# Kernel tuning notes

Hardware: AMD Instinct MI355X
Metric: run time of the kernel (lower is better)

Reference implementation:

```python
import jax, jax.numpy as jnp
import numpy as np

C = 192

def _dw_conv(x, w, k):
    # x: [B, C, H, W]; w: [C, 1, k, k]; depthwise => feature_group_count=C
    pad = k // 2
    return jax.lax.conv_general_dilated(
        x, w,
        window_strides=(1, 1),
        padding=[(pad, pad), (pad, pad)],
        dimension_numbers=("NCHW", "OIHW", "NCHW"),
        feature_group_count=x.shape[1],
    )

def setup_inputs() -> dict:
    key = jax.random.key(0)
    k1, k2, k3 = jax.random.split(key, 3)
    x = jax.random.normal(k1, (32, C, 64, 64), dtype=jnp.float32)
    # depthwise kernels: (out_ch=C, in_ch/groups=1, kh, kw), fan_in-style scaling
    w5 = jax.random.normal(k2, (C, 1, 5, 5), dtype=jnp.float32) * (1.0 / 5.0)
    w51 = jax.random.normal(k3, (C, 1, 51, 51), dtype=jnp.float32) * (1.0 / 51.0)
    return {"x": x, "w5": w5, "w51": w51}

def reference(x, w5, w51):
    # out = dw5(x) + dw51(x)
    return _dw_conv(x, w5, 5) + _dw_conv(x, w51, 51)
```

## Files before the change

kernel.cpp:

```cpp
#include <hip/hip_runtime.h>

typedef __bf16 bf16x8 __attribute__((ext_vector_type(8)));
typedef float  f32x16 __attribute__((ext_vector_type(16)));

__device__ __forceinline__ unsigned short f2bf_bits(float f) {
    unsigned int u = __builtin_bit_cast(unsigned int, f);
    u += 0x7FFFu + ((u >> 16) & 1u);
    return (unsigned short)(u >> 16);
}

__global__ void __launch_bounds__(512) dw5_51_kernel(
    const float* __restrict__ x,
    const float* __restrict__ w5,
    const float* __restrict__ w51,
    float* __restrict__ out)
{
    __shared__ unsigned short wlds[8 * 1024];
    __shared__ unsigned short rowbuf[8][2][1088];

    const int tid = threadIdx.x;
    const int wg  = blockIdx.x;
    const int c   = wg >> 2;
    const int bg  = wg & 3;

    {
        const int s   = tid >> 2;
        const int qtr = tid & 3;
        const int kh  = 88 - s;
        const bool rowok = (kh >= 0) && (kh <= 50);
        #pragma unroll
        for (int i = 0; i < 16; ++i) {
            const int kw = qtr * 16 + i;
            float v = 0.0f;
            if (rowok && kw <= 50) {
                v = w51[c * 2601 + kh * 51 + kw];
                if (kh >= 23 && kh < 28 && kw >= 23 && kw < 28)
                    v += w5[c * 25 + (kh - 23) * 5 + (kw - 23)];
            }
            wlds[(kw >> 3) * 1024 + s * 8 + (kw & 7)] = f2bf_bits(v);
        }
    }

    const int lane = tid & 63;
    const int wv   = tid >> 6;
    const int b    = bg * 8 + wv;
    const int n32  = lane & 31;
    const int gg   = lane >> 5;
    const int q    = lane & 7;
    const int u8   = n32 >> 3;

    {
        unsigned int* z = (unsigned int*)&rowbuf[wv][0][0];
        #pragma unroll
        for (int i = 0; i < 17; ++i) z[lane + 64 * i] = 0u;
    }
    __syncthreads();

    const long imgbase = ((long)b * 192 + c) * 4096;
    const float* xrow = x + imgbase + lane;
    float* outp = out + imgbase;

    const int bidx = 136 * q + 8 * u8 + 8 * gg;
    unsigned short* rb0 = &rowbuf[wv][0][0];
    unsigned short* rb1 = &rowbuf[wv][1][0];
    const int wbase = lane + 25;

    f32x16 acc00 = {}, acc01 = {}, acc10 = {}, acc11 = {};

    const int abase = gg * 1024 + n32 * 8;

    auto compute = [&](const unsigned short* __restrict__ rb, int r) {
        bf16x8 d[6];
        #pragma unroll
        for (int t = 0; t < 6; ++t) d[t] = *(const bf16x8*)&rb[bidx + 16 * t];
        if (r <= 56) {
            const int ai = abase + (63 - r) * 8;
            #pragma unroll
            for (int ks = 0; ks < 4; ++ks) {
                const bf16x8 Af = *(const bf16x8*)&wlds[ai + ks * 2048];
                acc00 = __builtin_amdgcn_mfma_f32_32x32x16_bf16(Af, d[ks],     acc00, 0, 0, 0);
                acc01 = __builtin_amdgcn_mfma_f32_32x32x16_bf16(Af, d[ks + 2], acc01, 0, 0, 0);
            }
        }
        if (r >= 7) {
            const int ai = abase + (95 - r) * 8;
            #pragma unroll
            for (int ks = 0; ks < 4; ++ks) {
                const bf16x8 Af = *(const bf16x8*)&wlds[ai + ks * 2048];
                acc10 = __builtin_amdgcn_mfma_f32_32x32x16_bf16(Af, d[ks],     acc10, 0, 0, 0);
                acc11 = __builtin_amdgcn_mfma_f32_32x32x16_bf16(Af, d[ks + 2], acc11, 0, 0, 0);
            }
        }
    };

    float xv = xrow[0];
    {
        const unsigned short xb = f2bf_bits(xv);
        #pragma unroll
        for (int qq = 0; qq < 8; ++qq) rb0[wbase + 135 * qq] = xb;
    }
    xv = xrow[64];

    #pragma unroll 1
    for (int rr = 0; rr < 64; rr += 2) {
        {
            const unsigned short xb = f2bf_bits(xv);
            #pragma unroll
            for (int qq = 0; qq < 8; ++qq) rb1[wbase + 135 * qq] = xb;
            if (rr + 2 < 64) xv = xrow[(rr + 2) * 64];
            compute(rb0, rr);
        }
        {
            if (rr + 2 < 64) {
                const unsigned short xb = f2bf_bits(xv);
                #pragma unroll
                for (int qq = 0; qq < 8; ++qq) rb0[wbase + 135 * qq] = xb;
                if (rr + 3 < 64) xv = xrow[(rr + 3) * 64];
            }
            compute(rb1, rr + 1);
        }
    }

    #pragma unroll
    for (int v = 0; v < 16; ++v) {
        const int ho = (v & 3) + 8 * (v >> 2) + 4 * gg;
        outp[ho * 64 + n32]             = acc00[v];
        outp[ho * 64 + n32 + 32]        = acc01[v];
        outp[(ho + 32) * 64 + n32]      = acc10[v];
        outp[(ho + 32) * 64 + n32 + 32] = acc11[v];
    }
}

extern "C" void kernel_launch(void* const* d_in, const int* in_sizes, int n_in,
                              void* d_out, int out_size, void* d_ws, size_t ws_size,
                              hipStream_t stream) {
    (void)in_sizes; (void)n_in; (void)d_ws; (void)ws_size; (void)out_size;
    const float* x   = (const float*)d_in[0];
    const float* w5  = (const float*)d_in[1];
    const float* w51 = (const float*)d_in[2];
    float* out = (float*)d_out;
    dim3 grid(192 * 4), block(512);
    hipLaunchKernelGGL(dw5_51_kernel, grid, block, 0, stream, x, w5, w51, out);
}
```

Baseline: 141.7 us.

## Process two images per wave to reuse LDS weight fragments across MFMAs

Each wave now handles two batch images instead of one, with 256-thread blocks covering the same 8 images per block. Weight A-fragments are loaded from LDS once per row and reused for both images' MFMAs, halving weight LDS reads per MFMA. The cost is doubled accumulator registers (128 floats per lane) and fewer waves per block, which may lower occupancy or cause spills.

Result: faster. 138.1 us (-2.5%).

```diff
diff --git a/kernel.cpp b/kernel.cpp
--- a/kernel.cpp
+++ b/kernel.cpp
@@ -9,14 +9,14 @@
     return (unsigned short)(u >> 16);
 }
 
-__global__ void __launch_bounds__(512) dw5_51_kernel(
+__global__ void __launch_bounds__(256, 2) dw5_51_kernel(
     const float* __restrict__ x,
     const float* __restrict__ w5,
     const float* __restrict__ w51,
     float* __restrict__ out)
 {
     __shared__ unsigned short wlds[8 * 1024];
-    __shared__ unsigned short rowbuf[8][2][1088];
+    __shared__ unsigned short rowbuf[4][2][2][1088];
 
     const int tid = threadIdx.x;
     const int wg  = blockIdx.x;
@@ -24,13 +24,13 @@
     const int bg  = wg & 3;
 
     {
-        const int s   = tid >> 2;
-        const int qtr = tid & 3;
-        const int kh  = 88 - s;
+        const int s    = tid >> 1;
+        const int half = tid & 1;
+        const int kh   = 88 - s;
         const bool rowok = (kh >= 0) && (kh <= 50);
         #pragma unroll
-        for (int i = 0; i < 16; ++i) {
-            const int kw = qtr * 16 + i;
+        for (int j = 0; j < 32; ++j) {
+            const int kw = half * 32 + j;
             float v = 0.0f;
             if (rowok && kw <= 50) {
                 v = w51[c * 2601 + kh * 51 + kw];
@@ -43,91 +43,122 @@
 
     const int lane = tid & 63;
     const int wv   = tid >> 6;
-    const int b    = bg * 8 + wv;
+    const int b0   = bg * 8 + wv * 2;
     const int n32  = lane & 31;
     const int gg   = lane >> 5;
     const int q    = lane & 7;
     const int u8   = n32 >> 3;
 
     {
-        unsigned int* z = (unsigned int*)&rowbuf[wv][0][0];
+        unsigned int* z = (unsigned int*)&rowbuf[wv][0][0][0];
         #pragma unroll
-        for (int i = 0; i < 17; ++i) z[lane + 64 * i] = 0u;
+        for (int i = 0; i < 34; ++i) z[lane + 64 * i] = 0u;
     }
     __syncthreads();
 
-    const long imgbase = ((long)b * 192 + c) * 4096;
-    const float* xrow = x + imgbase + lane;
-    float* outp = out + imgbase;
+    const long ib0 = ((long)b0 * 192 + c) * 4096;
+    const long ib1 = ((long)(b0 + 1) * 192 + c) * 4096;
+    const float* xr0 = x + ib0 + lane;
+    const float* xr1 = x + ib1 + lane;
+    float* outp0 = out + ib0;
+    float* outp1 = out + ib1;
 
     const int bidx = 136 * q + 8 * u8 + 8 * gg;
-    unsigned short* rb0 = &rowbuf[wv][0][0];
-    unsigned short* rb1 = &rowbuf[wv][1][0];
+    unsigned short* rbA0 = &rowbuf[wv][0][0][0];
+    unsigned short* rbA1 = &rowbuf[wv][0][1][0];
+    unsigned short* rbB0 = &rowbuf[wv][1][0][0];
+    unsigned short* rbB1 = &rowbuf[wv][1][1][0];
     const int wbase = lane + 25;
 
-    f32x16 acc00 = {}, acc01 = {}, acc10 = {}, acc11 = {};
-
+    f32x16 acc[2][2][2] = {};
     const int abase = gg * 1024 + n32 * 8;
 
-    auto compute = [&](const unsigned short* __restrict__ rb, int r) {
-        bf16x8 d[6];
-        #pragma unroll
-        for (int t = 0; t < 6; ++t) d[t] = *(const bf16x8*)&rb[bidx + 16 * t];
-        if (r <= 56) {
+    auto compute = [&](const unsigned short* __restrict__ rb0,
+                       const unsigned short* __restrict__ rb1, int r) {
+        const bool t0 = (r <= 56);
+        const bool t1 = (r >= 7);
+        bf16x8 A0[4], A1[4];
+        if (t0) {
             const int ai = abase + (63 - r) * 8;
             #pragma unroll
-            for (int ks = 0; ks < 4; ++ks) {
-                const bf16x8 Af = *(const bf16x8*)&wlds[ai + ks * 2048];
-                acc00 = __builtin_amdgcn_mfma_f32_32x32x16_bf16(Af, d[ks],     acc00, 0, 0, 0);
-                acc01 = __builtin_amdgcn_mfma_f32_32x32x16_bf16(Af, d[ks + 2], acc01, 0, 0, 0);
-            }
+            for (int ks = 0; ks < 4; ++ks) A0[ks] = *(const bf16x8*)&wlds[ai + ks * 2048];
         }
-        if (r >= 7) {
+        if (t1) {
             const int ai = abase + (95 - r) * 8;
             #pragma unroll
-            for (int ks = 0; ks < 4; ++ks) {
-                const bf16x8 Af = *(const bf16x8*)&wlds[ai + ks * 2048];
-                acc10 = __builtin_amdgcn_mfma_f32_32x32x16_bf16(Af, d[ks],     acc10, 0, 0, 0);
-                acc11 = __builtin_amdgcn_mfma_f32_32x32x16_bf16(Af, d[ks + 2], acc11, 0, 0, 0);
+            for (int ks = 0; ks < 4; ++ks) A1[ks] = *(const bf16x8*)&wlds[ai + ks * 2048];
+        }
+        const unsigned short* rbs[2] = { rb0, rb1 };
+        #pragma unroll
+        for (int img = 0; img < 2; ++img) {
+            bf16x8 d[6];
+            #pragma unroll
+            for (int t = 0; t < 6; ++t) d[t] = *(const bf16x8*)&rbs[img][bidx + 16 * t];
+            if (t0) {
+                #pragma unroll
+                for (int ks = 0; ks < 4; ++ks) {
+                    acc[img][0][0] = __builtin_amdgcn_mfma_f32_32x32x16_bf16(A0[ks], d[ks],     acc[img][0][0], 0, 0, 0);
+                    acc[img][0][1] = __builtin_amdgcn_mfma_f32_32x32x16_bf16(A0[ks], d[ks + 2], acc[img][0][1], 0, 0, 0);
+                }
+            }
+            if (t1) {
+                #pragma unroll
+                for (int ks = 0; ks < 4; ++ks) {
+                    acc[img][1][0] = __builtin_amdgcn_mfma_f32_32x32x16_bf16(A1[ks], d[ks],     acc[img][1][0], 0, 0, 0);
+                    acc[img][1][1] = __builtin_amdgcn_mfma_f32_32x32x16_bf16(A1[ks], d[ks + 2], acc[img][1][1], 0, 0, 0);
+                }
             }
         }
     };
 
-    float xv = xrow[0];
+    float xv0 = xr0[0], xv1 = xr1[0];
     {
-        const unsigned short xb = f2bf_bits(xv);
+        const unsigned short b0w = f2bf_bits(xv0), b1w = f2bf_bits(xv1);
         #pragma unroll
-        for (int qq = 0; qq < 8; ++qq) rb0[wbase + 135 * qq] = xb;
+        for (int qq = 0; qq < 8; ++qq) {
+            rbA0[wbase + 135 * qq] = b0w;
+            rbB0[wbase + 135 * qq] = b1w;
+        }
     }
-    xv = xrow[64];
+    xv0 = xr0[64]; xv1 = xr1[64];
 
     #pragma unroll 1
     for (int rr = 0; rr < 64; rr += 2) {
         {
-            const unsigned short xb = f2bf_bits(xv);
+            const unsigned short b0w = f2bf_bits(xv0), b1w = f2bf_bits(xv1);
             #pragma unroll
-            for (int qq = 0; qq < 8; ++qq) rb1[wbase + 135 * qq] = xb;
-            if (rr + 2 < 64) xv = xrow[(rr + 2) * 64];
-            compute(rb0, rr);
+            for (int qq = 0; qq < 8; ++qq) {
+                rbA1[wbase + 135 * qq] = b0w;
+                rbB1[wbase + 135 * qq] = b1w;
+            }
+            if (rr + 2 < 64) { xv0 = xr0[(rr + 2) * 64]; xv1 = xr1[(rr + 2) * 64]; }
+            compute(rbA0, rbB0, rr);
         }
         {
             if (rr + 2 < 64) {
-                const unsigned short xb = f2bf_bits(xv);
+                const unsigned short b0w = f2bf_bits(xv0), b1w = f2bf_bits(xv1);
                 #pragma unroll
-                for (int qq = 0; qq < 8; ++qq) rb0[wbase + 135 * qq] = xb;
-                if (rr + 3 < 64) xv = xrow[(rr + 3) * 64];
+                for (int qq = 0; qq < 8; ++qq) {
+                    rbA0[wbase + 135 * qq] = b0w;
+                    rbB0[wbase + 135 * qq] = b1w;
+                }
+                if (rr + 3 < 64) { xv0 = xr0[(rr + 3) * 64]; xv1 = xr1[(rr + 3) * 64]; }
             }
-            compute(rb1, rr + 1);
+            compute(rbA1, rbB1, rr + 1);
         }
     }
 
     #pragma unroll
     for (int v = 0; v < 16; ++v) {
         const int ho = (v & 3) + 8 * (v >> 2) + 4 * gg;
-        outp[ho * 64 + n32]             = acc00[v];
-        outp[ho * 64 + n32 + 32]        = acc01[v];
-        outp[(ho + 32) * 64 + n32]      = acc10[v];
-        outp[(ho + 32) * 64 + n32 + 32] = acc11[v];
+        outp0[ho * 64 + n32]             = acc[0][0][0][v];
+        outp0[ho * 64 + n32 + 32]        = acc[0][0][1][v];
+        outp0[(ho + 32) * 64 + n32]      = acc[0][1][0][v];
+        outp0[(ho + 32) * 64 + n32 + 32] = acc[0][1][1][v];
+        outp1[ho * 64 + n32]             = acc[1][0][0][v];
+        outp1[ho * 64 + n32 + 32]        = acc[1][0][1][v];
+        outp1[(ho + 32) * 64 + n32]      = acc[1][1][0][v];
+        outp1[(ho + 32) * 64 + n32 + 32] = acc[1][1][1][v];
     }
 }
 
@@ -139,6 +170,6 @@
     const float* w5  = (const float*)d_in[1];
     const float* w51 = (const float*)d_in[2];
     float* out = (float*)d_out;
-    dim3 grid(192 * 4), block(512);
+    dim3 grid(192 * 4), block(256);
     hipLaunchKernelGGL(dw5_51_kernel, grid, block, 0, stream, x, w5, w51, out);
 }
```

## Halve workgroup size and software-pipeline LDS operand loads ahead of MFMAs

Applied to the files above, without the earlier changes.

Workgroups shrink from 8 waves to 4 and the grid doubles to 1536 blocks, with launch bounds asking for two blocks per CU. This cuts per-block LDS and spreads work more evenly across CUs. The row loop is now double-buffered in registers: the next row's weight and input fragments are loaded from LDS while the current row's MFMAs run, and s_setprio raises priority around the MFMA bursts. The price is that each channel's weight tile is loaded and converted twice as often, and register pressure rises from holding two sets of A/B fragments.

Measured after the change: 153.9 us. 8.6% more time.

```diff
diff --git a/kernel.cpp b/kernel.cpp
--- a/kernel.cpp
+++ b/kernel.cpp
@@ -9,28 +9,28 @@
     return (unsigned short)(u >> 16);
 }
 
-__global__ void __launch_bounds__(512) dw5_51_kernel(
+__global__ void __launch_bounds__(256, 2) dw5_51_kernel(
     const float* __restrict__ x,
     const float* __restrict__ w5,
     const float* __restrict__ w51,
     float* __restrict__ out)
 {
     __shared__ unsigned short wlds[8 * 1024];
-    __shared__ unsigned short rowbuf[8][2][1088];
+    __shared__ unsigned short rowbuf[4][2][1088];
 
     const int tid = threadIdx.x;
     const int wg  = blockIdx.x;
-    const int c   = wg >> 2;
-    const int bg  = wg & 3;
+    const int c   = wg >> 3;
+    const int bg  = wg & 7;
 
     {
-        const int s   = tid >> 2;
-        const int qtr = tid & 3;
-        const int kh  = 88 - s;
+        const int s    = tid >> 1;
+        const int half = tid & 1;
+        const int kh   = 88 - s;
         const bool rowok = (kh >= 0) && (kh <= 50);
         #pragma unroll
-        for (int i = 0; i < 16; ++i) {
-            const int kw = qtr * 16 + i;
+        for (int j = 0; j < 32; ++j) {
+            const int kw = half * 32 + j;
             float v = 0.0f;
             if (rowok && kw <= 50) {
                 v = w51[c * 2601 + kh * 51 + kw];
@@ -43,7 +43,7 @@
 
     const int lane = tid & 63;
     const int wv   = tid >> 6;
-    const int b    = bg * 8 + wv;
+    const int b    = bg * 4 + wv;
     const int n32  = lane & 31;
     const int gg   = lane >> 5;
     const int q    = lane & 7;
@@ -60,64 +60,78 @@
     const float* xrow = x + imgbase + lane;
     float* outp = out + imgbase;
 
-    const int bidx = 136 * q + 8 * u8 + 8 * gg;
-    unsigned short* rb0 = &rowbuf[wv][0][0];
-    unsigned short* rb1 = &rowbuf[wv][1][0];
+    const int bidx  = 136 * q + 8 * u8 + 8 * gg;
     const int wbase = lane + 25;
+    const int abase = gg * 1024 + n32 * 8;
+
+    unsigned short* buf0 = &rowbuf[wv][0][0];
+    unsigned short* buf1 = &rowbuf[wv][1][0];
 
     f32x16 acc00 = {}, acc01 = {}, acc10 = {}, acc11 = {};
 
-    const int abase = gg * 1024 + n32 * 8;
-
-    auto compute = [&](const unsigned short* __restrict__ rb, int r) {
-        bf16x8 d[6];
+    auto loadA = [&](bf16x8 (&A)[8], int r) {
+        const int rc = r & 63;
+        const int s0 = (63 - rc) * 8 + abase;
+        const int s1 = (95 - rc) * 8 + abase;
         #pragma unroll
-        for (int t = 0; t < 6; ++t) d[t] = *(const bf16x8*)&rb[bidx + 16 * t];
+        for (int ks = 0; ks < 4; ++ks) {
+            A[ks]     = *(const bf16x8*)&wlds[s0 + ks * 2048];
+            A[4 + ks] = *(const bf16x8*)&wlds[s1 + ks * 2048];
+        }
+    };
+    auto loadB = [&](bf16x8 (&D)[6], const unsigned short* p) {
+        #pragma unroll
+        for (int t = 0; t < 6; ++t) D[t] = *(const bf16x8*)&p[bidx + 16 * t];
+    };
+    auto domfma = [&](bf16x8 (&A)[8], bf16x8 (&D)[6], int r) {
+        __builtin_amdgcn_s_setprio(1);
         if (r <= 56) {
-            const int ai = abase + (63 - r) * 8;
             #pragma unroll
             for (int ks = 0; ks < 4; ++ks) {
-                const bf16x8 Af = *(const bf16x8*)&wlds[ai + ks * 2048];
-                acc00 = __builtin_amdgcn_mfma_f32_32x32x16_bf16(Af, d[ks],     acc00, 0, 0, 0);
-                acc01 = __builtin_amdgcn_mfma_f32_32x32x16_bf16(Af, d[ks + 2], acc01, 0, 0, 0);
+                acc00 = __builtin_amdgcn_mfma_f32_32x32x16_bf16(A[ks], D[ks],     acc00, 0, 0, 0);
+                acc01 = __builtin_amdgcn_mfma_f32_32x32x16_bf16(A[ks], D[ks + 2], acc01, 0, 0, 0);
             }
         }
         if (r >= 7) {
-            const int ai = abase + (95 - r) * 8;
             #pragma unroll
             for (int ks = 0; ks < 4; ++ks) {
-                const bf16x8 Af = *(const bf16x8*)&wlds[ai + ks * 2048];
-                acc10 = __builtin_amdgcn_mfma_f32_32x32x16_bf16(Af, d[ks],     acc10, 0, 0, 0);
-                acc11 = __builtin_amdgcn_mfma_f32_32x32x16_bf16(Af, d[ks + 2], acc11, 0, 0, 0);
+                acc10 = __builtin_amdgcn_mfma_f32_32x32x16_bf16(A[4 + ks], D[ks],     acc10, 0, 0, 0);
+                acc11 = __builtin_amdgcn_mfma_f32_32x32x16_bf16(A[4 + ks], D[ks + 2], acc11, 0, 0, 0);
             }
         }
+        __builtin_amdgcn_s_setprio(0);
+    };
+    auto writerow = [&](unsigned short* p, float v) {
+        const unsigned short w0 = f2bf_bits(v);
+        #pragma unroll
+        for (int qq = 0; qq < 8; ++qq) p[wbase + 135 * qq] = w0;
     };
 
     float xv = xrow[0];
-    {
-        const unsigned short xb = f2bf_bits(xv);
-        #pragma unroll
-        for (int qq = 0; qq < 8; ++qq) rb0[wbase + 135 * qq] = xb;
-    }
+    writerow(buf0, xv);
     xv = xrow[64];
+    writerow(buf1, xv);
+    xv = xrow[128];
+
+    bf16x8 AE[8], AO[8], DE[6], DO[6];
+    loadA(AE, 0);
+    loadB(DE, buf0);
 
     #pragma unroll 1
     for (int rr = 0; rr < 64; rr += 2) {
-        {
-            const unsigned short xb = f2bf_bits(xv);
-            #pragma unroll
-            for (int qq = 0; qq < 8; ++qq) rb1[wbase + 135 * qq] = xb;
-            if (rr + 2 < 64) xv = xrow[(rr + 2) * 64];
-            compute(rb0, rr);
+        loadA(AO, rr + 1);
+        loadB(DO, buf1);
+        domfma(AE, DE, rr);
+        if (rr + 2 < 64) {
+            writerow(buf0, xv);
+            if (rr + 3 < 64) xv = xrow[(rr + 3) * 64];
         }
-        {
-            if (rr + 2 < 64) {
-                const unsigned short xb = f2bf_bits(xv);
-                #pragma unroll
-                for (int qq = 0; qq < 8; ++qq) rb0[wbase + 135 * qq] = xb;
-                if (rr + 3 < 64) xv = xrow[(rr + 3) * 64];
-            }
-            compute(rb1, rr + 1);
+        loadA(AE, rr + 2);
+        loadB(DE, buf0);
+        domfma(AO, DO, rr + 1);
+        if (rr + 3 < 64) {
+            writerow(buf1, xv);
+            if (rr + 4 < 64) xv = xrow[(rr + 4) * 64];
         }
     }
 
@@ -139,6 +153,6 @@
     const float* w5  = (const float*)d_in[1];
     const float* w51 = (const float*)d_in[2];
     float* out = (float*)d_out;
-    dim3 grid(192 * 4), block(512);
+    dim3 grid(192 * 8), block(256);
     hipLaunchKernelGGL(dw5_51_kernel, grid, block, 0, stream, x, w5, w51, out);
 }
```
